# Performance work log

Hardware: AMD Instinct MI355X
Metric: run time of the kernel (lower is better)

## Reference

```python
import jax, jax.numpy as jnp
import numpy as np

T, B, E, H = 2048, 4, 1024, 16
D = E // H  # head_dim = 64


def setup_inputs() -> dict:
    key = jax.random.key(0)
    k0, k1, k2 = jax.random.split(key, 3)
    std = (2.0 / (E + E)) ** 0.5  # matches reset_parameters
    inp = jax.random.normal(k0, (T, B, E), jnp.float32)
    in_w = jax.random.normal(k1, (3 * E, E), jnp.float32) * std
    in_b = jnp.zeros((3 * E,), jnp.float32)
    out_w = jax.random.normal(k2, (E, E), jnp.float32) * std
    out_b = jnp.zeros((E,), jnp.float32)
    # standard RoPE angle table, duplicated across halves so rotate_half pairing is exact
    inv_freq = 1.0 / (10000.0 ** (jnp.arange(0, D, 2, dtype=jnp.float32) / D))  # [D/2]
    ang = jnp.arange(T, dtype=jnp.float32)[:, None] * inv_freq[None, :]          # [T, D/2]
    pos = jnp.concatenate([ang, ang], axis=-1)                                    # [T, D]
    attn_mask = jnp.triu(jnp.ones((T, T), dtype=bool), k=1)  # True = masked (future)
    return {
        "input": inp,
        "pos": pos,
        "in_proj_weight": in_w,
        "in_proj_bias": in_b,
        "out_proj_weight": out_w,
        "out_proj_bias": out_b,
        "attn_mask": attn_mask,
    }


def _rotate_half(x):
    x1, x2 = jnp.split(x, 2, axis=-1)
    return jnp.concatenate([-x2, x1], axis=-1)


def reference(input, pos, in_proj_weight, in_proj_bias, out_proj_weight,
              out_proj_bias, attn_mask):
    Tq, Bq, Eq = input.shape
    nh = H
    hd = Eq // nh
    scaling = hd ** -0.5
    # fused QKV projection: [T,B,3E]
    qkv = input @ in_proj_weight.T + in_proj_bias
    q, k, v = jnp.split(qkv, 3, axis=-1)
    q = q.reshape(Tq, Bq, nh, hd)
    k = k.reshape(Tq, Bq, nh, hd)
    v = v.reshape(Tq, Bq, nh, hd)
    # rotary positional encoding applied inline to q and k
    cos = jnp.cos(pos)[:, None, None, :]  # [T,1,1,D]
    sin = jnp.sin(pos)[:, None, None, :]
    q = q * cos + _rotate_half(q) * sin
    k = k * cos + _rotate_half(k) * sin
    q = q * scaling
    # attention scores [B,H,T,S]
    scores = jnp.einsum('tbhd,sbhd->bhts', q, k)
    scores = jnp.where(attn_mask[None, None, :, :], -jnp.inf, scores)
    attn = jax.nn.softmax(scores, axis=-1)  # coverage
    ctx = jnp.einsum('bhts,sbhd->tbhd', attn, v).reshape(Tq, Bq, Eq)
    out = ctx @ out_proj_weight.T + out_proj_bias
    return out, attn
```

## Files before the change

kernel.cpp:

```cpp
#include <hip/hip_runtime.h>

typedef unsigned short u16;
typedef unsigned int u32;

#define TT 2048
#define BB 4
#define EE 1024
#define HH 16
#define DD 64
#define LOG2E 1.4426950408889634f

typedef __bf16 bf16x8 __attribute__((ext_vector_type(8)));
typedef float f32x4 __attribute__((ext_vector_type(4)));

__device__ __forceinline__ f32x4 mfma16(bf16x8 a, bf16x8 b, f32x4 c) {
  return __builtin_amdgcn_mfma_f32_16x16x32_bf16(a, b, c, 0, 0, 0);
}

__device__ __forceinline__ u16 f2bf(float f) {
  u32 u = __float_as_uint(f);
  u += 0x7fffu + ((u >> 16) & 1u);
  return (u16)(u >> 16);
}
__device__ __forceinline__ float bf2f(u16 u) {
  return __uint_as_float(((u32)u) << 16);
}

__device__ __forceinline__ void load_lds16(const void* g, void* l) {
  __builtin_amdgcn_global_load_lds((const __attribute__((address_space(1))) u32*)g,
                                   (__attribute__((address_space(3))) u32*)l, 16, 0, 0);
}

__global__ __launch_bounds__(256) void cvt_kernel(const float* __restrict__ in,
                                                  u16* __restrict__ out, int n4) {
  int i = blockIdx.x * 256 + threadIdx.x;
  if (i >= n4) return;
  float4 v = ((const float4*)in)[i];
  u32 lo = (u32)f2bf(v.x) | ((u32)f2bf(v.y) << 16);
  u32 hi = (u32)f2bf(v.z) | ((u32)f2bf(v.w) << 16);
  ((uint2*)out)[i] = make_uint2(lo, hi);
}

template<bool BF16_OUT>
__global__ __launch_bounds__(256) void gemm_bt(const u16* __restrict__ A,
    const u16* __restrict__ B, const float* __restrict__ bias,
    void* __restrict__ Cp, int M, int N, int K)
{
  __shared__ u16 As[128 * 32];
  __shared__ u16 Bs[128 * 32];
  const int tid = threadIdx.x;
  const int m0 = blockIdx.y * 128;
  const int n0 = blockIdx.x * 128;
  const int w = tid >> 6, lane = tid & 63;
  const int quad = lane >> 4, l16 = lane & 15;
  const int wm = (w & 1) * 64, wn = (w >> 1) * 64;

  const f32x4 zero4 = {0.f, 0.f, 0.f, 0.f};
  f32x4 acc[4][4];
#pragma unroll
  for (int i = 0; i < 4; i++)
#pragma unroll
    for (int j = 0; j < 4; j++) acc[i][j] = zero4;

  for (int k0 = 0; k0 < K; k0 += 32) {
#pragma unroll
    for (int i = 0; i < 2; i++) {
      int c = i * 256 + tid;
      int row = c >> 2, col = (c & 3) * 8;
      load_lds16(A + (size_t)(m0 + row) * K + k0 + col, &As[c * 8]);
      load_lds16(B + (size_t)(n0 + row) * K + k0 + col, &Bs[c * 8]);
    }
    __syncthreads();
    bf16x8 af[4], bfr[4];
#pragma unroll
    for (int i = 0; i < 4; i++)
      af[i] = *(const bf16x8*)&As[(wm + i * 16 + l16) * 32 + quad * 8];
#pragma unroll
    for (int j = 0; j < 4; j++)
      bfr[j] = *(const bf16x8*)&Bs[(wn + j * 16 + l16) * 32 + quad * 8];
#pragma unroll
    for (int i = 0; i < 4; i++)
#pragma unroll
      for (int j = 0; j < 4; j++)
        acc[i][j] = mfma16(af[i], bfr[j], acc[i][j]);
    __syncthreads();
  }
#pragma unroll
  for (int i = 0; i < 4; i++)
#pragma unroll
    for (int j = 0; j < 4; j++) {
      int col = n0 + wn + j * 16 + l16;
      float bv = bias[col];
#pragma unroll
      for (int r = 0; r < 4; r++) {
        int row = m0 + wm + i * 16 + quad * 4 + r;
        float v = acc[i][j][r] + bv;
        if (BF16_OUT) ((u16*)Cp)[(size_t)row * N + col] = f2bf(v);
        else          ((float*)Cp)[(size_t)row * N + col] = v;
      }
    }
}

__global__ __launch_bounds__(256) void rope_kernel(const u16* __restrict__ qkv,
    const float* __restrict__ pos, u16* __restrict__ Qg, u16* __restrict__ Kg)
{
  int u = blockIdx.x * 256 + threadIdx.x;
  int d0 = (u & 15) * 4;
  int h = (u >> 4) & 15;
  int m = u >> 8;
  int t = m >> 2, b = m & 3;
  const u16* rowq = qkv + (size_t)m * 3072 + h * 64;
  uint2 qa = *(const uint2*)(rowq + d0);
  uint2 qb = *(const uint2*)(rowq + (d0 ^ 32));
  uint2 ka = *(const uint2*)(rowq + 1024 + d0);
  uint2 kb = *(const uint2*)(rowq + 1024 + (d0 ^ 32));
  float qv[4] = {bf2f((u16)(qa.x & 0xffff)), bf2f((u16)(qa.x >> 16)),
                 bf2f((u16)(qa.y & 0xffff)), bf2f((u16)(qa.y >> 16))};
  float qp[4] = {bf2f((u16)(qb.x & 0xffff)), bf2f((u16)(qb.x >> 16)),
                 bf2f((u16)(qb.y & 0xffff)), bf2f((u16)(qb.y >> 16))};
  float kv[4] = {bf2f((u16)(ka.x & 0xffff)), bf2f((u16)(ka.x >> 16)),
                 bf2f((u16)(ka.y & 0xffff)), bf2f((u16)(ka.y >> 16))};
  float kp[4] = {bf2f((u16)(kb.x & 0xffff)), bf2f((u16)(kb.x >> 16)),
                 bf2f((u16)(kb.y & 0xffff)), bf2f((u16)(kb.y >> 16))};
  float sgn = (d0 < 32) ? -1.f : 1.f;
  float qo[4], ko[4];
#pragma unroll
  for (int i = 0; i < 4; i++) {
    float a = pos[t * 64 + d0 + i];
    float sv, cv;
    sincosf(a, &sv, &cv);
    qo[i] = (qv[i] * cv + sgn * qp[i] * sv) * 0.18033688f;
    ko[i] = kv[i] * cv + sgn * kp[i] * sv;
  }
  size_t obase = ((size_t)(b * 16 + h) * TT + t) * 64 + d0;
  *(uint2*)(Qg + obase) = make_uint2((u32)f2bf(qo[0]) | ((u32)f2bf(qo[1]) << 16),
                                     (u32)f2bf(qo[2]) | ((u32)f2bf(qo[3]) << 16));
  *(uint2*)(Kg + obase) = make_uint2((u32)f2bf(ko[0]) | ((u32)f2bf(ko[1]) << 16),
                                     (u32)f2bf(ko[2]) | ((u32)f2bf(ko[3]) << 16));
}

__global__ __launch_bounds__(256) void vtrans_kernel(const u16* __restrict__ qkv,
                                                     u16* __restrict__ Vt)
{
  __shared__ u16 Ls[64 * 64];
  int bh = blockIdx.y, b = bh >> 4, h = bh & 15;
  int t0 = blockIdx.x * 64;
  int tid = threadIdx.x;
#pragma unroll
  for (int i = 0; i < 2; i++) {
    int c = i * 256 + tid;
    int r = c >> 3, ch = c & 7;
    int m = (t0 + r) * 4 + b;
    uint4 v = *(const uint4*)(qkv + (size_t)m * 3072 + 2048 + h * 64 + ch * 8);
    *(uint4*)&Ls[r * 64 + ((ch ^ (r & 7)) * 8)] = v;
  }
  __syncthreads();
#pragma unroll
  for (int i = 0; i < 2; i++) {
    int u = i * 256 + tid;
    int d = u >> 3, tc = u & 7;
    u32 pk[4];
#pragma unroll
    for (int p = 0; p < 4; p++) {
      int r0 = tc * 8 + p * 2, r1 = r0 + 1;
      u16 a = Ls[r0 * 64 + (((d >> 3) ^ (r0 & 7)) * 8) + (d & 7)];
      u16 bb = Ls[r1 * 64 + (((d >> 3) ^ (r1 & 7)) * 8) + (d & 7)];
      pk[p] = (u32)a | ((u32)bb << 16);
    }
    *(uint4*)(Vt + ((size_t)bh * 64 + d) * TT + t0 + tc * 8) =
        make_uint4(pk[0], pk[1], pk[2], pk[3]);
  }
}

__global__ __launch_bounds__(256, 3) void attn_kernel(const u16* __restrict__ Qg,
    const u16* __restrict__ Kg, const u16* __restrict__ Vt,
    float* __restrict__ attn, u16* __restrict__ ctx)
{
  __shared__ u16 sm[24576];
  u16* QP = sm + 16384;

  const int bh = blockIdx.y;
  const int qt = (int)gridDim.x - 1 - (int)blockIdx.x;
  const int b = bh >> 4, h = bh & 15;
  const int q0 = qt * 128;
  const int tid = threadIdx.x;
  const int w = tid >> 6, lane = tid & 63;
  const int quad = lane >> 4, l16 = lane & 15;
  const f32x4 zero4 = {0.f, 0.f, 0.f, 0.f};

  const u16* Kbase = Kg + (size_t)bh * TT * 64;
  const u16* Vbase = Vt + (size_t)bh * 64 * TT;

  auto stageK128 = [&](int buf, int kt) {
    const u16* src = Kbase + (size_t)kt * 128 * 64;
    u16* dst = sm + buf * 8192;
#pragma unroll
    for (int i = 0; i < 4; i++) {
      int c = i * 256 + tid;
      int row = c >> 3, chl = c & 7;
      load_lds16(src + row * 64 + ((chl ^ (row & 7)) * 8), dst + c * 8);
    }
  };
  auto stageK64 = [&](int buf, int kt) {
    const u16* src = Kbase + (size_t)kt * 64 * 64;
    u16* dst = sm + buf * 4096;
#pragma unroll
    for (int i = 0; i < 2; i++) {
      int c = i * 256 + tid;
      int row = c >> 3, chl = c & 7;
      load_lds16(src + row * 64 + ((chl ^ (row & 7)) * 8), dst + c * 8);
    }
  };
  auto stageV64 = [&](int buf, int kt) {
    const u16* src = Vbase + kt * 64;
    u16* dst = sm + 8192 + buf * 4096;
#pragma unroll
    for (int i = 0; i < 2; i++) {
      int c = i * 256 + tid;
      int d = c >> 3, chl = c & 7;
      load_lds16(src + (size_t)d * TT + ((chl ^ (d & 7)) * 8), dst + c * 8);
    }
  };

  {
    const u16* src = Qg + ((size_t)bh * TT + q0) * 64;
#pragma unroll
    for (int i = 0; i < 4; i++) {
      int c = i * 256 + tid;
      int row = c >> 3, chl = c & 7;
      load_lds16(src + row * 64 + ((chl ^ (row & 7)) * 8), &QP[c * 8]);
    }
  }
  stageK128(0, 0);
  __syncthreads();

  bf16x8 aq[2][2];
#pragma unroll
  for (int i = 0; i < 2; i++)
#pragma unroll
    for (int ks = 0; ks < 2; ks++) {
      int row = w * 32 + i * 16 + l16;
      int ch = (ks * 4 + quad) ^ (row & 7);
      aq[i][ks] = *(const bf16x8*)&QP[row * 64 + ch * 8];
    }

  float mrow[8], lrow[8];
#pragma unroll
  for (int x = 0; x < 8; x++) { mrow[x] = -1e30f; lrow[x] = 0.f; }

  int cur = 0;
  for (int kt = 0; kt <= qt; kt++) {
    if (kt < qt) stageK128(cur ^ 1, kt + 1);
    const u16* Ks = sm + cur * 8192;
    f32x4 sacc[2][8];
#pragma unroll
    for (int i = 0; i < 2; i++)
#pragma unroll
      for (int j = 0; j < 8; j++) sacc[i][j] = zero4;
#pragma unroll
    for (int ks = 0; ks < 2; ks++)
#pragma unroll
      for (int j = 0; j < 8; j++) {
        int row = j * 16 + l16;
        int ch = (ks * 4 + quad) ^ (row & 7);
        bf16x8 bk = *(const bf16x8*)&Ks[row * 64 + ch * 8];
        sacc[0][j] = mfma16(aq[0][ks], bk, sacc[0][j]);
        sacc[1][j] = mfma16(aq[1][ks], bk, sacc[1][j]);
      }
    if (kt == qt) {
#pragma unroll
      for (int i = 0; i < 2; i++)
#pragma unroll
        for (int j = 0; j < 8; j++) {
          int scol = j * 16 + l16;
#pragma unroll
          for (int r = 0; r < 4; r++) {
            int trow = w * 32 + i * 16 + quad * 4 + r;
            if (scol > trow) sacc[i][j][r] = -1e30f;
          }
        }
    }
#pragma unroll
    for (int i = 0; i < 2; i++)
#pragma unroll
      for (int r = 0; r < 4; r++) {
        int idx = i * 4 + r;
        float a0 = fmaxf(sacc[i][0][r], sacc[i][1][r]);
        float a1 = fmaxf(sacc[i][2][r], sacc[i][3][r]);
        float a2 = fmaxf(sacc[i][4][r], sacc[i][5][r]);
        float a3 = fmaxf(sacc[i][6][r], sacc[i][7][r]);
        float mx = fmaxf(fmaxf(a0, a1), fmaxf(a2, a3));
        float mnew = fmaxf(mrow[idx], mx);
        float s = 0.f;
#pragma unroll
        for (int j = 0; j < 8; j++) s += exp2f(sacc[i][j][r] - mnew);
        lrow[idx] = lrow[idx] * exp2f(mrow[idx] - mnew) + s;
        mrow[idx] = mnew;
      }
    __syncthreads();
    cur ^= 1;
  }

  float inv_l[8];
#pragma unroll
  for (int idx = 0; idx < 8; idx++) {
    float m = mrow[idx], l = lrow[idx];
#pragma unroll
    for (int off = 1; off < 16; off <<= 1) {
      float mo = __shfl_xor(m, off);
      float lo = __shfl_xor(l, off);
      float mn = fmaxf(m, mo);
      l = l * exp2f(m - mn) + lo * exp2f(mo - mn);
      m = mn;
    }
    mrow[idx] = m;
    inv_l[idx] = 1.f / l;
  }

  f32x4 cacc[2][4];
#pragma unroll
  for (int i = 0; i < 2; i++)
#pragma unroll
    for (int j = 0; j < 4; j++) cacc[i][j] = zero4;

  const int KT = 2 * (qt + 1);
  stageK64(0, 0);
  stageV64(0, 0);
  __syncthreads();
  cur = 0;
  for (int kt = 0; kt < KT; kt++) {
    if (kt < KT - 1) { stageK64(cur ^ 1, kt + 1); stageV64(cur ^ 1, kt + 1); }
    const u16* Ks = sm + cur * 4096;
    const u16* Vs = sm + 8192 + cur * 4096;
    f32x4 sacc[2][4];
#pragma unroll
    for (int i = 0; i < 2; i++)
#pragma unroll
      for (int j = 0; j < 4; j++) sacc[i][j] = zero4;
#pragma unroll
    for (int ks = 0; ks < 2; ks++)
#pragma unroll
      for (int j = 0; j < 4; j++) {
        int row = j * 16 + l16;
        int ch = (ks * 4 + quad) ^ (row & 7);
        bf16x8 bk = *(const bf16x8*)&Ks[row * 64 + ch * 8];
        sacc[0][j] = mfma16(aq[0][ks], bk, sacc[0][j]);
        sacc[1][j] = mfma16(aq[1][ks], bk, sacc[1][j]);
      }
    if (kt >= KT - 2) {
      int off = kt * 64 - q0;
#pragma unroll
      for (int i = 0; i < 2; i++)
#pragma unroll
        for (int j = 0; j < 4; j++) {
          int scol = j * 16 + l16;
#pragma unroll
          for (int r = 0; r < 4; r++) {
            int tl = w * 32 + i * 16 + quad * 4 + r;
            if (off + scol > tl) sacc[i][j][r] = -1e30f;
          }
        }
    }
    float* abase = attn + ((size_t)bh * TT + q0) * TT + kt * 64;
#pragma unroll
    for (int i = 0; i < 2; i++)
#pragma unroll
      for (int j = 0; j < 4; j++) {
#pragma unroll
        for (int r = 0; r < 4; r++) {
          int tr = w * 32 + i * 16 + quad * 4 + r;
          float p = exp2f(sacc[i][j][r] - mrow[i * 4 + r]) * inv_l[i * 4 + r];
          abase[(size_t)tr * TT + j * 16 + l16] = p;
          int sc = j * 16 + l16;
          QP[tr * 64 + (((sc >> 3) ^ (tr & 7)) * 8) + (sc & 7)] = f2bf(p);
        }
      }
#pragma unroll
    for (int ks2 = 0; ks2 < 2; ks2++) {
      bf16x8 ap[2];
#pragma unroll
      for (int i = 0; i < 2; i++) {
        int row = w * 32 + i * 16 + l16;
        int ch = (ks2 * 4 + quad) ^ (row & 7);
        ap[i] = *(const bf16x8*)&QP[row * 64 + ch * 8];
      }
#pragma unroll
      for (int j = 0; j < 4; j++) {
        int drow = j * 16 + l16;
        int ch = (ks2 * 4 + quad) ^ (drow & 7);
        bf16x8 bv = *(const bf16x8*)&Vs[drow * 64 + ch * 8];
        cacc[0][j] = mfma16(ap[0], bv, cacc[0][j]);
        cacc[1][j] = mfma16(ap[1], bv, cacc[1][j]);
      }
    }
    __syncthreads();
    cur ^= 1;
  }

#pragma unroll
  for (int i = 0; i < 2; i++)
#pragma unroll
    for (int j = 0; j < 4; j++)
#pragma unroll
      for (int r = 0; r < 4; r++) {
        int tr = q0 + w * 32 + i * 16 + quad * 4 + r;
        int d = j * 16 + l16;
        ctx[((size_t)tr * BB + b) * EE + h * 64 + d] = f2bf(cacc[i][j][r]);
      }

  int nz4 = (15 - qt) * 32;
  if (nz4 > 0) {
    float4 z = make_float4(0.f, 0.f, 0.f, 0.f);
    float* base = attn + ((size_t)bh * TT + q0) * TT + (qt + 1) * 128;
    for (int r = 0; r < 128; r++)
      for (int c4 = tid; c4 < nz4; c4 += 256)
        *(float4*)(base + (size_t)r * TT + c4 * 4) = z;
  }
}

extern "C" void kernel_launch(void* const* d_in, const int* in_sizes, int n_in,
                              void* d_out, int out_size, void* d_ws, size_t ws_size,
                              hipStream_t stream) {
  (void)in_sizes; (void)n_in; (void)out_size; (void)ws_size;
  const float* input = (const float*)d_in[0];
  const float* pos   = (const float*)d_in[1];
  const float* in_w  = (const float*)d_in[2];
  const float* in_b  = (const float*)d_in[3];
  const float* out_w = (const float*)d_in[4];
  const float* out_b = (const float*)d_in[5];

  float* out  = (float*)d_out;
  float* attn = out + (size_t)TT * BB * EE;

  char* ws = (char*)d_ws;
  u16* inA = (u16*)ws;
  u16* w1b = (u16*)(ws + 16777216);
  u16* w2b = (u16*)(ws + 23068672);
  u16* Qg  = (u16*)(ws + 25165824);
  u16* Kg  = (u16*)(ws + 41943040);
  u16* Vt  = (u16*)(ws + 58720256);
  u16* ctx = inA;
  u16* qkv = (u16*)attn;

  cvt_kernel<<<8192, 256, 0, stream>>>(input, inA, 2097152);
  cvt_kernel<<<3072, 256, 0, stream>>>(in_w, w1b, 786432);
  cvt_kernel<<<1024, 256, 0, stream>>>(out_w, w2b, 262144);
  gemm_bt<true><<<dim3(24, 64), 256, 0, stream>>>(inA, w1b, in_b, (void*)qkv,
                                                  8192, 3072, 1024);
  rope_kernel<<<8192, 256, 0, stream>>>(qkv, pos, Qg, Kg);
  vtrans_kernel<<<dim3(32, 64), 256, 0, stream>>>(qkv, Vt);
  attn_kernel<<<dim3(16, 64), 256, 0, stream>>>(Qg, Kg, Vt, attn, ctx);
  gemm_bt<false><<<dim3(8, 64), 256, 0, stream>>>(ctx, w2b, out_b, (void*)out,
                                                  8192, 1024, 1024);
}
```

Baseline: 1.660 ms.

## Halve attention query tile to 64 rows and swizzle GEMM block order across XCDs

The attention kernel now processes 64 query rows per block instead of 128, doubling the grid to 2048 blocks. It also shrinks LDS use and raises the occupancy hint to 4 blocks per CU, which is meant to improve load balance across the causal triangle and keep more waves resident. Separately, the GEMM remaps block IDs so consecutive workgroups land on the same XCD, aiming at better L2 reuse. The trade-off is that each K/V tile is reused by fewer query rows, so K/V staging traffic per unit of work doubles.

```diff
diff --git a/kernel.cpp b/kernel.cpp
--- a/kernel.cpp
+++ b/kernel.cpp
@@ -49,8 +49,12 @@
   __shared__ u16 As[128 * 32];
   __shared__ u16 Bs[128 * 32];
   const int tid = threadIdx.x;
-  const int m0 = blockIdx.y * 128;
-  const int n0 = blockIdx.x * 128;
+  const int nbx = gridDim.x;
+  const int nwg = nbx * gridDim.y;
+  int orig = blockIdx.y * nbx + blockIdx.x;
+  int wg = (orig & 7) * (nwg >> 3) + (orig >> 3);
+  const int m0 = (wg / nbx) * 128;
+  const int n0 = (wg % nbx) * 128;
   const int w = tid >> 6, lane = tid & 63;
   const int quad = lane >> 4, l16 = lane & 15;
   const int wm = (w & 1) * 64, wn = (w >> 1) * 64;
@@ -172,17 +176,17 @@
   }
 }
 
-__global__ __launch_bounds__(256, 3) void attn_kernel(const u16* __restrict__ Qg,
+__global__ __launch_bounds__(256, 4) void attn_kernel(const u16* __restrict__ Qg,
     const u16* __restrict__ Kg, const u16* __restrict__ Vt,
     float* __restrict__ attn, u16* __restrict__ ctx)
 {
-  __shared__ u16 sm[24576];
+  __shared__ u16 sm[20480];
   u16* QP = sm + 16384;
 
   const int bh = blockIdx.y;
   const int qt = (int)gridDim.x - 1 - (int)blockIdx.x;
   const int b = bh >> 4, h = bh & 15;
-  const int q0 = qt * 128;
+  const int q0 = qt * 64;
   const int tid = threadIdx.x;
   const int w = tid >> 6, lane = tid & 63;
   const int quad = lane >> 4, l16 = lane & 15;
@@ -191,8 +195,8 @@
   const u16* Kbase = Kg + (size_t)bh * TT * 64;
   const u16* Vbase = Vt + (size_t)bh * 64 * TT;
 
-  auto stageK128 = [&](int buf, int kt) {
-    const u16* src = Kbase + (size_t)kt * 128 * 64;
+  auto stageK128 = [&](int buf, int kt2) {
+    const u16* src = Kbase + (size_t)kt2 * 128 * 64;
     u16* dst = sm + buf * 8192;
 #pragma unroll
     for (int i = 0; i < 4; i++) {
@@ -225,7 +229,7 @@
   {
     const u16* src = Qg + ((size_t)bh * TT + q0) * 64;
 #pragma unroll
-    for (int i = 0; i < 4; i++) {
+    for (int i = 0; i < 2; i++) {
       int c = i * 256 + tid;
       int row = c >> 3, chl = c & 7;
       load_lds16(src + row * 64 + ((chl ^ (row & 7)) * 8), &QP[c * 8]);
@@ -234,29 +238,26 @@
   stageK128(0, 0);
   __syncthreads();
 
-  bf16x8 aq[2][2];
-#pragma unroll
-  for (int i = 0; i < 2; i++)
-#pragma unroll
-    for (int ks = 0; ks < 2; ks++) {
-      int row = w * 32 + i * 16 + l16;
-      int ch = (ks * 4 + quad) ^ (row & 7);
-      aq[i][ks] = *(const bf16x8*)&QP[row * 64 + ch * 8];
-    }
-
-  float mrow[8], lrow[8];
-#pragma unroll
-  for (int x = 0; x < 8; x++) { mrow[x] = -1e30f; lrow[x] = 0.f; }
-
+  bf16x8 aq[2];
+#pragma unroll
+  for (int ks = 0; ks < 2; ks++) {
+    int row = w * 16 + l16;
+    int ch = (ks * 4 + quad) ^ (row & 7);
+    aq[ks] = *(const bf16x8*)&QP[row * 64 + ch * 8];
+  }
+
+  float mrow[4], lrow[4];
+#pragma unroll
+  for (int x = 0; x < 4; x++) { mrow[x] = -1e30f; lrow[x] = 0.f; }
+
+  const int nk1 = (qt >> 1) + 1;
   int cur = 0;
-  for (int kt = 0; kt <= qt; kt++) {
-    if (kt < qt) stageK128(cur ^ 1, kt + 1);
+  for (int kt = 0; kt < nk1; kt++) {
+    if (kt < nk1 - 1) stageK128(cur ^ 1, kt + 1);
     const u16* Ks = sm + cur * 8192;
-    f32x4 sacc[2][8];
-#pragma unroll
-    for (int i = 0; i < 2; i++)
-#pragma unroll
-      for (int j = 0; j < 8; j++) sacc[i][j] = zero4;
+    f32x4 sacc[8];
+#pragma unroll
+    for (int j = 0; j < 8; j++) sacc[j] = zero4;
 #pragma unroll
     for (int ks = 0; ks < 2; ks++)
 #pragma unroll
@@ -264,46 +265,40 @@
         int row = j * 16 + l16;
         int ch = (ks * 4 + quad) ^ (row & 7);
         bf16x8 bk = *(const bf16x8*)&Ks[row * 64 + ch * 8];
-        sacc[0][j] = mfma16(aq[0][ks], bk, sacc[0][j]);
-        sacc[1][j] = mfma16(aq[1][ks], bk, sacc[1][j]);
-      }
-    if (kt == qt) {
-#pragma unroll
-      for (int i = 0; i < 2; i++)
-#pragma unroll
-        for (int j = 0; j < 8; j++) {
-          int scol = j * 16 + l16;
-#pragma unroll
-          for (int r = 0; r < 4; r++) {
-            int trow = w * 32 + i * 16 + quad * 4 + r;
-            if (scol > trow) sacc[i][j][r] = -1e30f;
-          }
+        sacc[j] = mfma16(aq[ks], bk, sacc[j]);
+      }
+    if (kt == nk1 - 1) {
+#pragma unroll
+      for (int j = 0; j < 8; j++) {
+        int scol = kt * 128 + j * 16 + l16;
+#pragma unroll
+        for (int r = 0; r < 4; r++) {
+          int trow = q0 + w * 16 + quad * 4 + r;
+          if (scol > trow) sacc[j][r] = -1e30f;
         }
-    }
-#pragma unroll
-    for (int i = 0; i < 2; i++)
-#pragma unroll
-      for (int r = 0; r < 4; r++) {
-        int idx = i * 4 + r;
-        float a0 = fmaxf(sacc[i][0][r], sacc[i][1][r]);
-        float a1 = fmaxf(sacc[i][2][r], sacc[i][3][r]);
-        float a2 = fmaxf(sacc[i][4][r], sacc[i][5][r]);
-        float a3 = fmaxf(sacc[i][6][r], sacc[i][7][r]);
-        float mx = fmaxf(fmaxf(a0, a1), fmaxf(a2, a3));
-        float mnew = fmaxf(mrow[idx], mx);
-        float s = 0.f;
-#pragma unroll
-        for (int j = 0; j < 8; j++) s += exp2f(sacc[i][j][r] - mnew);
-        lrow[idx] = lrow[idx] * exp2f(mrow[idx] - mnew) + s;
-        mrow[idx] = mnew;
-      }
+      }
+    }
+#pragma unroll
+    for (int r = 0; r < 4; r++) {
+      float a0 = fmaxf(sacc[0][r], sacc[1][r]);
+      float a1 = fmaxf(sacc[2][r], sacc[3][r]);
+      float a2 = fmaxf(sacc[4][r], sacc[5][r]);
+      float a3 = fmaxf(sacc[6][r], sacc[7][r]);
+      float mx = fmaxf(fmaxf(a0, a1), fmaxf(a2, a3));
+      float mnew = fmaxf(mrow[r], mx);
+      float s = 0.f;
+#pragma unroll
+      for (int j = 0; j < 8; j++) s += exp2f(sacc[j][r] - mnew);
+      lrow[r] = lrow[r] * exp2f(mrow[r] - mnew) + s;
+      mrow[r] = mnew;
+    }
     __syncthreads();
     cur ^= 1;
   }
 
-  float inv_l[8];
-#pragma unroll
-  for (int idx = 0; idx < 8; idx++) {
+  float inv_l[4];
+#pragma unroll
+  for (int idx = 0; idx < 4; idx++) {
     float m = mrow[idx], l = lrow[idx];
 #pragma unroll
     for (int off = 1; off < 16; off <<= 1) {
@@ -317,26 +312,22 @@
     inv_l[idx] = 1.f / l;
   }
 
-  f32x4 cacc[2][4];
-#pragma unroll
-  for (int i = 0; i < 2; i++)
-#pragma unroll
-    for (int j = 0; j < 4; j++) cacc[i][j] = zero4;
-
-  const int KT = 2 * (qt + 1);
+  f32x4 cacc[4];
+#pragma unroll
+  for (int j = 0; j < 4; j++) cacc[j] = zero4;
+
+  const int nk2 = qt + 1;
   stageK64(0, 0);
   stageV64(0, 0);
   __syncthreads();
   cur = 0;
-  for (int kt = 0; kt < KT; kt++) {
-    if (kt < KT - 1) { stageK64(cur ^ 1, kt + 1); stageV64(cur ^ 1, kt + 1); }
+  for (int kt = 0; kt < nk2; kt++) {
+    if (kt < nk2 - 1) { stageK64(cur ^ 1, kt + 1); stageV64(cur ^ 1, kt + 1); }
     const u16* Ks = sm + cur * 4096;
     const u16* Vs = sm + 8192 + cur * 4096;
-    f32x4 sacc[2][4];
-#pragma unroll
-    for (int i = 0; i < 2; i++)
-#pragma unroll
-      for (int j = 0; j < 4; j++) sacc[i][j] = zero4;
+    f32x4 sacc[4];
+#pragma unroll
+    for (int j = 0; j < 4; j++) sacc[j] = zero4;
 #pragma unroll
     for (int ks = 0; ks < 2; ks++)
 #pragma unroll
@@ -344,53 +335,45 @@
         int row = j * 16 + l16;
         int ch = (ks * 4 + quad) ^ (row & 7);
         bf16x8 bk = *(const bf16x8*)&Ks[row * 64 + ch * 8];
-        sacc[0][j] = mfma16(aq[0][ks], bk, sacc[0][j]);
-        sacc[1][j] = mfma16(aq[1][ks], bk, sacc[1][j]);
-      }
-    if (kt >= KT - 2) {
-      int off = kt * 64 - q0;
-#pragma unroll
-      for (int i = 0; i < 2; i++)
-#pragma unroll
-        for (int j = 0; j < 4; j++) {
-          int scol = j * 16 + l16;
-#pragma unroll
-          for (int r = 0; r < 4; r++) {
-            int tl = w * 32 + i * 16 + quad * 4 + r;
-            if (off + scol > tl) sacc[i][j][r] = -1e30f;
-          }
+        sacc[j] = mfma16(aq[ks], bk, sacc[j]);
+      }
+    if (kt == nk2 - 1) {
+#pragma unroll
+      for (int j = 0; j < 4; j++) {
+        int scol = j * 16 + l16;
+#pragma unroll
+        for (int r = 0; r < 4; r++) {
+          int tl = w * 16 + quad * 4 + r;
+          if (scol > tl) sacc[j][r] = -1e30f;
         }
+      }
     }
     float* abase = attn + ((size_t)bh * TT + q0) * TT + kt * 64;
 #pragma unroll
-    for (int i = 0; i < 2; i++)
-#pragma unroll
-      for (int j = 0; j < 4; j++) {
-#pragma unroll
-        for (int r = 0; r < 4; r++) {
-          int tr = w * 32 + i * 16 + quad * 4 + r;
-          float p = exp2f(sacc[i][j][r] - mrow[i * 4 + r]) * inv_l[i * 4 + r];
-          abase[(size_t)tr * TT + j * 16 + l16] = p;
-          int sc = j * 16 + l16;
-          QP[tr * 64 + (((sc >> 3) ^ (tr & 7)) * 8) + (sc & 7)] = f2bf(p);
-        }
-      }
+    for (int j = 0; j < 4; j++) {
+#pragma unroll
+      for (int r = 0; r < 4; r++) {
+        int tr = w * 16 + quad * 4 + r;
+        float p = exp2f(sacc[j][r] - mrow[r]) * inv_l[r];
+        abase[(size_t)tr * TT + j * 16 + l16] = p;
+        int sc = j * 16 + l16;
+        QP[tr * 64 + (((sc >> 3) ^ (tr & 7)) * 8) + (sc & 7)] = f2bf(p);
+      }
+    }
 #pragma unroll
     for (int ks2 = 0; ks2 < 2; ks2++) {
-      bf16x8 ap[2];
-#pragma unroll
-      for (int i = 0; i < 2; i++) {
-        int row = w * 32 + i * 16 + l16;
+      bf16x8 ap;
+      {
+        int row = w * 16 + l16;
         int ch = (ks2 * 4 + quad) ^ (row & 7);
-        ap[i] = *(const bf16x8*)&QP[row * 64 + ch * 8];
+        ap = *(const bf16x8*)&QP[row * 64 + ch * 8];
       }
 #pragma unroll
       for (int j = 0; j < 4; j++) {
         int drow = j * 16 + l16;
         int ch = (ks2 * 4 + quad) ^ (drow & 7);
         bf16x8 bv = *(const bf16x8*)&Vs[drow * 64 + ch * 8];
-        cacc[0][j] = mfma16(ap[0], bv, cacc[0][j]);
-        cacc[1][j] = mfma16(ap[1], bv, cacc[1][j]);
+        cacc[j] = mfma16(ap, bv, cacc[j]);
       }
     }
     __syncthreads();
@@ -398,21 +381,19 @@
   }
 
 #pragma unroll
-  for (int i = 0; i < 2; i++)
-#pragma unroll
-    for (int j = 0; j < 4; j++)
-#pragma unroll
-      for (int r = 0; r < 4; r++) {
-        int tr = q0 + w * 32 + i * 16 + quad * 4 + r;
-        int d = j * 16 + l16;
-        ctx[((size_t)tr * BB + b) * EE + h * 64 + d] = f2bf(cacc[i][j][r]);
-      }
-
-  int nz4 = (15 - qt) * 32;
+  for (int j = 0; j < 4; j++)
+#pragma unroll
+    for (int r = 0; r < 4; r++) {
+      int tr = q0 + w * 16 + quad * 4 + r;
+      int d = j * 16 + l16;
+      ctx[((size_t)tr * BB + b) * EE + h * 64 + d] = f2bf(cacc[j][r]);
+    }
+
+  int nz4 = (31 - qt) * 16;
   if (nz4 > 0) {
     float4 z = make_float4(0.f, 0.f, 0.f, 0.f);
-    float* base = attn + ((size_t)bh * TT + q0) * TT + (qt + 1) * 128;
-    for (int r = 0; r < 128; r++)
+    float* base = attn + ((size_t)bh * TT + q0) * TT + (qt + 1) * 64;
+    for (int r = 0; r < 64; r++)
       for (int c4 = tid; c4 < nz4; c4 += 256)
         *(float4*)(base + (size_t)r * TT + c4 * 4) = z;
   }
@@ -449,7 +430,7 @@
                                                   8192, 3072, 1024);
   rope_kernel<<<8192, 256, 0, stream>>>(qkv, pos, Qg, Kg);
   vtrans_kernel<<<dim3(32, 64), 256, 0, stream>>>(qkv, Vt);
-  attn_kernel<<<dim3(16, 64), 256, 0, stream>>>(Qg, Kg, Vt, attn, ctx);
+  attn_kernel<<<dim3(32, 64), 256, 0, stream>>>(Qg, Kg, Vt, attn, ctx);
   gemm_bt<false><<<dim3(8, 64), 256, 0, stream>>>(ctx, w2b, out_b, (void*)out,
                                                   8192, 1024, 1024);
 }
```

Measured after the change: 1.385 ms. 16.6% less time.
